# Kernel optimization log

Hardware: AMD Instinct MI355X
Metric: run time of the kernel (lower is better)

Reference implementation:

```python
import jax, jax.numpy as jnp
import numpy as np

B, S, D, H = 2, 2048, 1024, 16
HD = D // H

def setup_inputs() -> dict:
    key = jax.random.key(0)
    ks = jax.random.split(key, 9)
    scale = 1.0 / np.sqrt(D)
    return {
        "query": jax.random.normal(ks[0], (B, S, D), jnp.float32),
        "key":   jax.random.normal(ks[1], (B, S, D), jnp.float32),
        "value": jax.random.normal(ks[2], (B, S, D), jnp.float32),
        "Wq_w": jax.random.normal(ks[3], (D, D), jnp.float32) * scale,
        "Wq_b": jax.random.normal(ks[4], (D,), jnp.float32) * scale,
        "Wk_w": jax.random.normal(ks[5], (D, D), jnp.float32) * scale,
        "Wk_b": jax.random.normal(ks[6], (D,), jnp.float32) * scale,
        "Wv_w": jax.random.normal(ks[7], (D, D), jnp.float32) * scale,
        "Wv_b": jax.random.normal(ks[8], (D,), jnp.float32) * scale,
    }

def reference(query, key, value, Wq_w, Wq_b, Wk_w, Wk_b, Wv_w, Wv_b):
    b, s, d = query.shape
    # torch Linear: y = x @ W.T + b
    Q = query @ Wq_w.T + Wq_b
    K = key   @ Wk_w.T + Wk_b
    V = value @ Wv_w.T + Wv_b
    # [B, H, S, HD]
    Q = Q.reshape(b, -1, H, HD).transpose(0, 2, 1, 3)
    K = K.reshape(b, -1, H, HD).transpose(0, 2, 1, 3)
    V = V.reshape(b, -1, H, HD).transpose(0, 2, 1, 3)
    scores = jnp.einsum("bhqd,bhkd->bhqk", Q, K) / jnp.sqrt(jnp.float32(HD))
    attn = jax.nn.softmax(scores, axis=-1)
    context = jnp.einsum("bhqk,bhkd->bhqd", attn, V)  # [B,H,S,HD]
    attn_output = context.transpose(0, 2, 1, 3).reshape(b, -1, H * HD)  # [B,S,D]
    return (context, attn_output)
```

## Files before the change

### kernel.cpp

```cpp
#include <hip/hip_runtime.h>
#include <hip/hip_bf16.h>

constexpr int Bb = 2, Ss = 2048, Dd = 1024, Hh = 16, HD = 64;
constexpr int Mrows = Bb * Ss;
constexpr float QSCALE = 0.125f * 1.44269504088896f;
constexpr size_t CTX_ELEMS = (size_t)Bb * Hh * Ss * HD;

typedef __attribute__((ext_vector_type(8)))  short        short8;
typedef __attribute__((ext_vector_type(4)))  float        floatx4;
typedef __attribute__((ext_vector_type(16))) float        floatx16;
typedef __attribute__((ext_vector_type(4)))  unsigned int uintx4;
typedef __attribute__((ext_vector_type(8)))  __bf16       bf16x8;

#define DEVI __device__ __forceinline__

DEVI unsigned short f2bf(float f) {
  union { float f; unsigned u; } x; x.f = f;
  return (unsigned short)((x.u + 0x7fffu + ((x.u >> 16) & 1u)) >> 16);
}
DEVI float fexp2(float x) {
#if __has_builtin(__builtin_amdgcn_exp2f)
  return __builtin_amdgcn_exp2f(x);
#else
  return __expf(x * 0.6931471805599453f);
#endif
}
DEVI unsigned int cvtpk(float lo, float hi) {
  unsigned int r;
  asm("v_cvt_pk_bf16_f32 %0, %1, %2" : "=v"(r) : "v"(lo), "v"(hi));
  return r;
}

constexpr size_t XE = (size_t)Mrows * Dd;
constexpr size_t WE = (size_t)Dd * Dd;
constexpr size_t OFF_O = 3 * WE;

__global__ __launch_bounds__(256) void convert_w(
    const float* __restrict__ wq, const float* __restrict__ wk, const float* __restrict__ wv,
    unsigned short* __restrict__ dst)
{
  const int sel = blockIdx.y;
  const float* src = sel == 0 ? wq : sel == 1 ? wk : wv;
  unsigned short* d = dst + (size_t)sel * WE;
  const size_t stride = (size_t)gridDim.x * blockDim.x;
  for (size_t i = (size_t)blockIdx.x * blockDim.x + threadIdx.x; i < WE / 8; i += stride) {
    const floatx4 a = *(const floatx4*)(src + i * 8);
    const floatx4 b = *(const floatx4*)(src + i * 8 + 4);
    uintx4 o;
    o[0] = cvtpk(a[0], a[1]); o[1] = cvtpk(a[2], a[3]);
    o[2] = cvtpk(b[0], b[1]); o[3] = cvtpk(b[2], b[3]);
    *(uintx4*)(d + i * 8) = o;
  }
}

template<bool SWAP>
DEVI void store_out(floatx4 (&acc)[4][4], const float* __restrict__ bias,
                    unsigned short* __restrict__ out, float oscale,
                    int bm, int bn, int wm, int wn, int lrow, int lg)
{
  if constexpr (!SWAP) {
    #pragma unroll
    for (int ni = 0; ni < 4; ++ni) {
      const int gcol = bn * 128 + wn + ni * 16 + lrow;
      const float bval = bias[gcol];
      const int h = gcol >> 6, hd = gcol & 63;
      #pragma unroll
      for (int mi = 0; mi < 4; ++mi)
        #pragma unroll
        for (int r = 0; r < 4; ++r) {
          const int grow = bm * 128 + wm + mi * 16 + lg * 4 + r;
          const int b = grow >> 11, s = grow & 2047;
          out[(((size_t)(b * Hh + h) * Ss + s) << 6) + hd] = f2bf((acc[mi][ni][r] + bval) * oscale);
        }
    }
  } else {
    #pragma unroll
    for (int ni = 0; ni < 4; ++ni)
      #pragma unroll
      for (int r = 0; r < 4; ++r) {
        const int n = bn * 128 + wn + ni * 16 + lg * 4 + r;
        const float bval = bias[n];
        #pragma unroll
        for (int mi = 0; mi < 4; ++mi) {
          const int m = bm * 128 + wm + mi * 16 + lrow;
          out[(size_t)n * Mrows + m] = f2bf(acc[mi][ni][r] + bval);
        }
      }
  }
}

DEVI void gload16(const unsigned short* g, unsigned short* l) {
  __builtin_amdgcn_global_load_lds(
      (const __attribute__((address_space(1))) unsigned int*)g,
      (__attribute__((address_space(3))) unsigned int*)l, 16, 0, 0);
}

template<bool SWAP>
DEVI void gemm_core_mixed(const float* __restrict__ X,
                          const unsigned short* __restrict__ W,
                          const float* __restrict__ bias,
                          unsigned short* __restrict__ out, float oscale,
                          unsigned short* As, unsigned short* Bs, int bm, int bn)
{
  const int t = threadIdx.x, wid = t >> 6, lane = t & 63;
  const int lrow = lane & 15, lg = lane >> 4;
  const int wm = (wid >> 1) * 64, wn = (wid & 1) * 64;

  const int ar = t >> 2;
  const int acb = (t & 3) * 16;
  const float* gAbase = X + (size_t)(bm * 128 + ar) * Dd + acb;

  const int srow = lane >> 3;
  const int gch  = (lane & 7) ^ srow;
  const unsigned short* gB = W + (size_t)(bn * 128 + wid * 32 + srow) * Dd + gch * 8;
  unsigned short* lB = Bs + wid * 4 * 512;

  floatx4 ra[2][4];
  auto loadA = [&](int k0) {
    #pragma unroll
    for (int i = 0; i < 2; ++i)
      #pragma unroll
      for (int j = 0; j < 4; ++j)
        ra[i][j] = *(const floatx4*)(gAbase + (size_t)i * 64 * Dd + k0 + j * 4);
  };
  auto writeA = [&]() {
    #pragma unroll
    for (int i = 0; i < 2; ++i) {
      const int row = ar + i * 64;
      #pragma unroll
      for (int j2 = 0; j2 < 2; ++j2) {
        const floatx4 a = ra[i][2 * j2], b = ra[i][2 * j2 + 1];
        uintx4 w;
        w[0] = cvtpk(a[0], a[1]); w[1] = cvtpk(a[2], a[3]);
        w[2] = cvtpk(b[0], b[1]); w[3] = cvtpk(b[2], b[3]);
        const int cc = (acb >> 3) + j2;
        *(uintx4*)&As[row * 64 + ((cc ^ (row & 7)) << 3)] = w;
      }
    }
  };

  floatx4 acc[4][4];
  #pragma unroll
  for (int i = 0; i < 4; ++i)
    #pragma unroll
    for (int j = 0; j < 4; ++j) acc[i][j] = 0.0f;

  loadA(0);

  for (int k0 = 0; k0 < Dd; k0 += 64) {
    __syncthreads();
    writeA();
    #pragma unroll
    for (int j = 0; j < 4; ++j)
      gload16(gB + (size_t)j * 8 * Dd + k0, lB + j * 512);
    __syncthreads();
    if (k0 + 64 < Dd) loadA(k0 + 64);

    #pragma unroll
    for (int kf = 0; kf < 2; ++kf) {
      bf16x8 af[4], bf[4];
      #pragma unroll
      for (int mi = 0; mi < 4; ++mi) {
        const int row = wm + mi * 16 + lrow;
        const int ch  = ((kf << 2) | lg) ^ (lrow & 7);
        af[mi] = __builtin_bit_cast(bf16x8, *(const short8*)&As[row * 64 + (ch << 3)]);
      }
      #pragma unroll
      for (int ni = 0; ni < 4; ++ni) {
        const int row = wn + ni * 16 + lrow;
        const int ch  = ((kf << 2) | lg) ^ (lrow & 7);
        bf[ni] = __builtin_bit_cast(bf16x8, *(const short8*)&Bs[row * 64 + (ch << 3)]);
      }
      #pragma unroll
      for (int mi = 0; mi < 4; ++mi)
        #pragma unroll
        for (int ni = 0; ni < 4; ++ni) {
          if constexpr (SWAP)
            acc[mi][ni] = __builtin_amdgcn_mfma_f32_16x16x32_bf16(bf[ni], af[mi], acc[mi][ni], 0, 0, 0);
          else
            acc[mi][ni] = __builtin_amdgcn_mfma_f32_16x16x32_bf16(af[mi], bf[ni], acc[mi][ni], 0, 0, 0);
        }
    }
  }
  store_out<SWAP>(acc, bias, out, oscale, bm, bn, wm, wn, lrow, lg);
}

__global__ __launch_bounds__(256, 3) void qkv_gemm(
    const float* __restrict__ q, const float* __restrict__ k, const float* __restrict__ v,
    const unsigned short* __restrict__ wbf,
    const float* __restrict__ bq, const float* __restrict__ bk, const float* __restrict__ bv,
    unsigned short* __restrict__ outbase)
{
  __shared__ __align__(16) unsigned short As[128 * 64];
  __shared__ __align__(16) unsigned short Bs[128 * 64];

  const int id  = blockIdx.y * 256 + blockIdx.x;
  const int swz = (id & 7) * 96 + (id >> 3);
  const int sel = swz >> 8;
  const int bx  = swz & 255;
  const int bm = bx >> 3, bn = bx & 7;

  const float* X = sel == 0 ? q : sel == 1 ? k : v;
  const unsigned short* W = wbf + (size_t)sel * WE;
  const float* bias = sel == 0 ? bq : sel == 1 ? bk : bv;
  unsigned short* out = outbase + (size_t)sel * XE;

  if (sel == 2) gemm_core_mixed<true >(X, W, bias, out, 1.0f, As, Bs, bm, bn);
  else          gemm_core_mixed<false>(X, W, bias, out, sel == 0 ? QSCALE : 1.0f, As, Bs, bm, bn);
}

__global__ __launch_bounds__(512, 4) void attn_fwd8(
    const unsigned short* __restrict__ Qw, const unsigned short* __restrict__ Kw,
    const unsigned short* __restrict__ Vw, float* __restrict__ out)
{
  __shared__ __align__(16) char smemRaw[65536];
  unsigned short* KsB = (unsigned short*)smemRaw;
  unsigned short* VtB = (unsigned short*)(smemRaw + 32768);
  float* ctxL  = (float*)smemRaw;
  float* lsumL = (float*)(smemRaw + 32768);

  const int id  = blockIdx.y * 16 + blockIdx.x;
  const int swz = (id & 7) * 64 + (id >> 3);
  const int qb  = swz & 15, bh = swz >> 4;
  const int b   = bh >> 4, h = bh & 15;

  const int t = threadIdx.x, wid8 = t >> 6, lane = t & 63;
  const int kh = wid8 >> 2, wid = wid8 & 3;
  const int l31 = lane & 31, hi = lane >> 5;
  const int kvbase = kh << 10;
  const unsigned short* Qb = Qw + (size_t)bh * (Ss * HD);
  const unsigned short* Kb = Kw + (size_t)bh * (Ss * HD);
  const unsigned short* Vg = Vw + (size_t)(h * 64) * Mrows + b * Ss;
  const int q0 = qb * 128 + wid * 32;

  bf16x8 qf[4];
  #pragma unroll
  for (int hs = 0; hs < 4; ++hs)
    qf[hs] = __builtin_bit_cast(bf16x8,
        *(const short8*)(Qb + (size_t)(q0 + l31) * 64 + hs * 16 + hi * 8));

  floatx16 ctx[2];
  ctx[0] = 0.0f; ctx[1] = 0.0f;
  float lsumv = 0.0f;

  const int rl = lane >> 3;
  const int cs = (lane & 7) ^ rl;
  auto stage = [&](int T) {
    const int kv0 = kvbase + T * 64;
    unsigned short* Kd = KsB + (size_t)(kh * 2 + (T & 1)) * 4096;
    unsigned short* Vd = VtB + (size_t)(kh * 2 + (T & 1)) * 4096;
    #pragma unroll
    for (int i = 0; i < 2; ++i) {
      const int row = wid * 16 + i * 8 + rl;
      gload16(Kb + (size_t)(kv0 + row) * 64 + cs * 8, Kd + (wid * 16 + i * 8) * 64);
      gload16(Vg + (size_t)row * Mrows + kv0 + cs * 8, Vd + (wid * 16 + i * 8) * 64);
    }
  };

  stage(0);

  for (int it = 0; it < 16; ++it) {
    const int cur = it & 1;
    __syncthreads();
    if (it + 1 < 16) stage(it + 1);
    const unsigned short* Kc = KsB + (size_t)(kh * 2 + cur) * 4096;
    const unsigned short* Vc = VtB + (size_t)(kh * 2 + cur) * 4096;

    #pragma unroll
    for (int kvb = 0; kvb < 2; ++kvb) {
      floatx16 s = 0.0f;
      __builtin_amdgcn_s_setprio(1);
      #pragma unroll
      for (int hs = 0; hs < 4; ++hs) {
        const int ch = ((hs << 1) | hi) ^ (l31 & 7);
        const bf16x8 kf = __builtin_bit_cast(bf16x8,
            *(const short8*)&Kc[(kvb * 32 + l31) * 64 + (ch << 3)]);
        s = __builtin_amdgcn_mfma_f32_32x32x16_bf16(kf, qf[hs], s, 0, 0, 0);
      }
      __builtin_amdgcn_s_setprio(0);

      float p[16];
      #pragma unroll
      for (int r = 0; r < 16; ++r) { p[r] = fexp2(s[r]); lsumv += p[r]; }
      unsigned int c[8];
      #pragma unroll
      for (int i = 0; i < 8; ++i)
        asm("v_cvt_pk_bf16_f32 %0, %1, %2" : "=v"(c[i]) : "v"(p[2 * i]), "v"(p[2 * i + 1]));

      #pragma unroll
      for (int ks2 = 0; ks2 < 2; ++ks2) {
        unsigned int w0 = c[4 * ks2 + 0], w2 = c[4 * ks2 + 2];
        unsigned int w1 = c[4 * ks2 + 1], w3 = c[4 * ks2 + 3];
        asm("v_permlane32_swap_b32 %0, %1" : "+v"(w0), "+v"(w2));
        asm("v_permlane32_swap_b32 %0, %1" : "+v"(w1), "+v"(w3));
        uintx4 paw; paw[0] = w0; paw[1] = w1; paw[2] = w2; paw[3] = w3;
        const bf16x8 pa = __builtin_bit_cast(bf16x8, paw);

        const int ks = kvb * 2 + ks2;
        __builtin_amdgcn_s_setprio(1);
        #pragma unroll
        for (int nb = 0; nb < 2; ++nb) {
          const int ch = ((ks << 1) | hi) ^ (l31 & 7);
          const bf16x8 vf = __builtin_bit_cast(bf16x8,
              *(const short8*)&Vc[(nb * 32 + l31) * 64 + (ch << 3)]);
          ctx[nb] = __builtin_amdgcn_mfma_f32_32x32x16_bf16(pa, vf, ctx[nb], 0, 0, 0);
        }
        __builtin_amdgcn_s_setprio(0);
      }
    }
  }

  float sa = lsumv, sb = lsumv;
  asm("v_permlane32_swap_b32 %0, %1" : "+v"(sa), "+v"(sb));
  const float tot = lsumv + (hi ? sa : sb);

  __syncthreads();
  if (kh == 1) {
    #pragma unroll
    for (int r = 0; r < 16; ++r)
      #pragma unroll
      for (int nb = 0; nb < 2; ++nb)
        ctxL[(nb * 16 + r) * 256 + wid * 64 + lane] = ctx[nb][r];
    if (hi == 0) lsumL[wid * 32 + l31] = tot;
  }
  __syncthreads();
  if (kh == 0) {
    if (hi == 0) lsumL[128 + wid * 32 + l31] = tot + lsumL[wid * 32 + l31];
    #pragma unroll
    for (int r = 0; r < 16; ++r) {
      const int wr = (r & 3) + 8 * (r >> 2) + 4 * hi;
      const float inv = 1.0f / lsumL[128 + wid * 32 + wr];
      const int qrow = q0 + wr;
      #pragma unroll
      for (int nb = 0; nb < 2; ++nb) {
        const int hd = nb * 32 + l31;
        const float val = (ctx[nb][r] + ctxL[(nb * 16 + r) * 256 + wid * 64 + lane]) * inv;
        out[((size_t)bh * Ss + qrow) * 64 + hd] = val;
        out[CTX_ELEMS + (((size_t)(b * Ss + qrow)) << 10) + (h << 6) + hd] = val;
      }
    }
  }
}

extern "C" void kernel_launch(void* const* d_in, const int* in_sizes, int n_in,
                              void* d_out, int out_size, void* d_ws, size_t ws_size,
                              hipStream_t stream) {
  const float* q  = (const float*)d_in[0];
  const float* k  = (const float*)d_in[1];
  const float* v  = (const float*)d_in[2];
  const float* wq = (const float*)d_in[3];
  const float* bq = (const float*)d_in[4];
  const float* wk = (const float*)d_in[5];
  const float* bk = (const float*)d_in[6];
  const float* wv = (const float*)d_in[7];
  const float* bv = (const float*)d_in[8];
  unsigned short* ws = (unsigned short*)d_ws;
  float* out = (float*)d_out;

  unsigned short* wsW = ws;
  unsigned short* wsO = ws + OFF_O;

  convert_w<<<dim3(64, 3), 256, 0, stream>>>(wq, wk, wv, wsW);
  qkv_gemm<<<dim3(256, 3), 256, 0, stream>>>(q, k, v, wsW, bq, bk, bv, wsO);
  attn_fwd8<<<dim3(16, 32), 512, 0, stream>>>(wsO, wsO + XE, wsO + 2 * XE, out);
}
```

Measured before the change: 89.76 us.

## Pre-convert activations to bf16 and split attention KV into four quarters

The convert kernel now casts the q/k/v activations to bf16 along with the weights, so the QKV GEMM can load both operands straight into LDS with async global_load_lds instead of loading fp32 and converting in registers. The attention kernel now handles 64 query rows per block with four KV-quarter wave pairs, uses smaller LDS tiles (single-buffered K, double-buffered V) and a four-way reduction at the end, and launches twice as many blocks with a higher occupancy hint. This trades an extra full pass over the activations in the convert step for a simpler GEMM inner loop and more parallelism in attention.

```diff
diff --git a/kernel.cpp b/kernel.cpp
--- a/kernel.cpp
+++ b/kernel.cpp
@@ -25,31 +25,36 @@
   return __expf(x * 0.6931471805599453f);
 #endif
 }
-DEVI unsigned int cvtpk(float lo, float hi) {
-  unsigned int r;
-  asm("v_cvt_pk_bf16_f32 %0, %1, %2" : "=v"(r) : "v"(lo), "v"(hi));
-  return r;
-}
 
 constexpr size_t XE = (size_t)Mrows * Dd;
 constexpr size_t WE = (size_t)Dd * Dd;
-constexpr size_t OFF_O = 3 * WE;
-
-__global__ __launch_bounds__(256) void convert_w(
+constexpr size_t OFF_W = 3 * XE;
+constexpr size_t OFF_O = 3 * XE + 3 * WE;
+
+__global__ __launch_bounds__(256) void convert_bf16(
+    const float* __restrict__ q, const float* __restrict__ k, const float* __restrict__ v,
     const float* __restrict__ wq, const float* __restrict__ wk, const float* __restrict__ wv,
     unsigned short* __restrict__ dst)
 {
   const int sel = blockIdx.y;
-  const float* src = sel == 0 ? wq : sel == 1 ? wk : wv;
-  unsigned short* d = dst + (size_t)sel * WE;
+  const float* src; size_t n, off;
+  switch (sel) {
+    case 0:  src = q;  n = XE; off = 0;            break;
+    case 1:  src = k;  n = XE; off = XE;           break;
+    case 2:  src = v;  n = XE; off = 2 * XE;       break;
+    case 3:  src = wq; n = WE; off = OFF_W;        break;
+    case 4:  src = wk; n = WE; off = OFF_W + WE;   break;
+    default: src = wv; n = WE; off = OFF_W + 2*WE; break;
+  }
+  unsigned short* d = dst + off;
   const size_t stride = (size_t)gridDim.x * blockDim.x;
-  for (size_t i = (size_t)blockIdx.x * blockDim.x + threadIdx.x; i < WE / 8; i += stride) {
+  for (size_t i = (size_t)blockIdx.x * blockDim.x + threadIdx.x; i < n / 8; i += stride) {
     const floatx4 a = *(const floatx4*)(src + i * 8);
     const floatx4 b = *(const floatx4*)(src + i * 8 + 4);
-    uintx4 o;
-    o[0] = cvtpk(a[0], a[1]); o[1] = cvtpk(a[2], a[3]);
-    o[2] = cvtpk(b[0], b[1]); o[3] = cvtpk(b[2], b[3]);
-    *(uintx4*)(d + i * 8) = o;
+    short8 o;
+    #pragma unroll
+    for (int j = 0; j < 4; ++j) { o[j] = (short)f2bf(a[j]); o[4 + j] = (short)f2bf(b[j]); }
+    *(short8*)(d + i * 8) = o;
   }
 }
 
@@ -96,48 +101,22 @@
 }
 
 template<bool SWAP>
-DEVI void gemm_core_mixed(const float* __restrict__ X,
-                          const unsigned short* __restrict__ W,
-                          const float* __restrict__ bias,
-                          unsigned short* __restrict__ out, float oscale,
-                          unsigned short* As, unsigned short* Bs, int bm, int bn)
+DEVI void gemm_core_bf16(const unsigned short* __restrict__ X,
+                         const unsigned short* __restrict__ W,
+                         const float* __restrict__ bias,
+                         unsigned short* __restrict__ out, float oscale,
+                         unsigned short* As, unsigned short* Bs, int bm, int bn)
 {
   const int t = threadIdx.x, wid = t >> 6, lane = t & 63;
   const int lrow = lane & 15, lg = lane >> 4;
   const int wm = (wid >> 1) * 64, wn = (wid & 1) * 64;
 
-  const int ar = t >> 2;
-  const int acb = (t & 3) * 16;
-  const float* gAbase = X + (size_t)(bm * 128 + ar) * Dd + acb;
-
   const int srow = lane >> 3;
   const int gch  = (lane & 7) ^ srow;
+  const unsigned short* gA = X + (size_t)(bm * 128 + wid * 32 + srow) * Dd + gch * 8;
   const unsigned short* gB = W + (size_t)(bn * 128 + wid * 32 + srow) * Dd + gch * 8;
+  unsigned short* lA = As + wid * 4 * 512;
   unsigned short* lB = Bs + wid * 4 * 512;
-
-  floatx4 ra[2][4];
-  auto loadA = [&](int k0) {
-    #pragma unroll
-    for (int i = 0; i < 2; ++i)
-      #pragma unroll
-      for (int j = 0; j < 4; ++j)
-        ra[i][j] = *(const floatx4*)(gAbase + (size_t)i * 64 * Dd + k0 + j * 4);
-  };
-  auto writeA = [&]() {
-    #pragma unroll
-    for (int i = 0; i < 2; ++i) {
-      const int row = ar + i * 64;
-      #pragma unroll
-      for (int j2 = 0; j2 < 2; ++j2) {
-        const floatx4 a = ra[i][2 * j2], b = ra[i][2 * j2 + 1];
-        uintx4 w;
-        w[0] = cvtpk(a[0], a[1]); w[1] = cvtpk(a[2], a[3]);
-        w[2] = cvtpk(b[0], b[1]); w[3] = cvtpk(b[2], b[3]);
-        const int cc = (acb >> 3) + j2;
-        *(uintx4*)&As[row * 64 + ((cc ^ (row & 7)) << 3)] = w;
-      }
-    }
-  };
 
   floatx4 acc[4][4];
   #pragma unroll
@@ -145,16 +124,14 @@
     #pragma unroll
     for (int j = 0; j < 4; ++j) acc[i][j] = 0.0f;
 
-  loadA(0);
-
   for (int k0 = 0; k0 < Dd; k0 += 64) {
     __syncthreads();
-    writeA();
-    #pragma unroll
-    for (int j = 0; j < 4; ++j)
+    #pragma unroll
+    for (int j = 0; j < 4; ++j) {
+      gload16(gA + (size_t)j * 8 * Dd + k0, lA + j * 512);
       gload16(gB + (size_t)j * 8 * Dd + k0, lB + j * 512);
+    }
     __syncthreads();
-    if (k0 + 64 < Dd) loadA(k0 + 64);
 
     #pragma unroll
     for (int kf = 0; kf < 2; ++kf) {
@@ -185,9 +162,8 @@
   store_out<SWAP>(acc, bias, out, oscale, bm, bn, wm, wn, lrow, lg);
 }
 
-__global__ __launch_bounds__(256, 3) void qkv_gemm(
-    const float* __restrict__ q, const float* __restrict__ k, const float* __restrict__ v,
-    const unsigned short* __restrict__ wbf,
+__global__ __launch_bounds__(256, 3) void qkv_gemm_bf16(
+    const unsigned short* __restrict__ ws,
     const float* __restrict__ bq, const float* __restrict__ bk, const float* __restrict__ bv,
     unsigned short* __restrict__ outbase)
 {
@@ -200,38 +176,40 @@
   const int bx  = swz & 255;
   const int bm = bx >> 3, bn = bx & 7;
 
-  const float* X = sel == 0 ? q : sel == 1 ? k : v;
-  const unsigned short* W = wbf + (size_t)sel * WE;
+  const unsigned short* X = ws + (size_t)sel * XE;
+  const unsigned short* W = ws + OFF_W + (size_t)sel * WE;
   const float* bias = sel == 0 ? bq : sel == 1 ? bk : bv;
   unsigned short* out = outbase + (size_t)sel * XE;
 
-  if (sel == 2) gemm_core_mixed<true >(X, W, bias, out, 1.0f, As, Bs, bm, bn);
-  else          gemm_core_mixed<false>(X, W, bias, out, sel == 0 ? QSCALE : 1.0f, As, Bs, bm, bn);
-}
-
-__global__ __launch_bounds__(512, 4) void attn_fwd8(
+  if (sel == 2) gemm_core_bf16<true >(X, W, bias, out, 1.0f,   As, Bs, bm, bn);
+  else          gemm_core_bf16<false>(X, W, bias, out, sel == 0 ? QSCALE : 1.0f, As, Bs, bm, bn);
+}
+
+__global__ __launch_bounds__(512, 6) void attn_fwd8(
     const unsigned short* __restrict__ Qw, const unsigned short* __restrict__ Kw,
     const unsigned short* __restrict__ Vw, float* __restrict__ out)
 {
-  __shared__ __align__(16) char smemRaw[65536];
-  unsigned short* KsB = (unsigned short*)smemRaw;
-  unsigned short* VtB = (unsigned short*)(smemRaw + 32768);
-  float* ctxL  = (float*)smemRaw;
-  float* lsumL = (float*)(smemRaw + 32768);
-
-  const int id  = blockIdx.y * 16 + blockIdx.x;
-  const int swz = (id & 7) * 64 + (id >> 3);
-  const int qb  = swz & 15, bh = swz >> 4;
+  __shared__ __align__(16) char smemRaw[50176];
+  float* ctxF  = (float*)smemRaw;
+  float* lsumQ = (float*)(smemRaw + 49152);
+  float* lsumC = (float*)(smemRaw + 49152 + 768);
+
+  const int id  = blockIdx.y * 32 + blockIdx.x;
+  const int swz = (id & 7) * 128 + (id >> 3);
+  const int qb  = swz & 31, bh = swz >> 5;
   const int b   = bh >> 4, h = bh & 15;
 
   const int t = threadIdx.x, wid8 = t >> 6, lane = t & 63;
-  const int kh = wid8 >> 2, wid = wid8 & 3;
+  const int kq = wid8 >> 1, wid = wid8 & 1;
   const int l31 = lane & 31, hi = lane >> 5;
-  const int kvbase = kh << 10;
+  const int kvbase = kq << 9;
   const unsigned short* Qb = Qw + (size_t)bh * (Ss * HD);
   const unsigned short* Kb = Kw + (size_t)bh * (Ss * HD);
   const unsigned short* Vg = Vw + (size_t)(h * 64) * Mrows + b * Ss;
-  const int q0 = qb * 128 + wid * 32;
+  const int q0 = qb * 64 + wid * 32;
+
+  unsigned short* Kq = (unsigned short*)(smemRaw + kq * 4096);
+  unsigned short* Vq = (unsigned short*)(smemRaw + 16384 + kq * 8192);
 
   bf16x8 qf[4];
   #pragma unroll
@@ -245,68 +223,77 @@
 
   const int rl = lane >> 3;
   const int cs = (lane & 7) ^ rl;
-  auto stage = [&](int T) {
-    const int kv0 = kvbase + T * 64;
-    unsigned short* Kd = KsB + (size_t)(kh * 2 + (T & 1)) * 4096;
-    unsigned short* Vd = VtB + (size_t)(kh * 2 + (T & 1)) * 4096;
+  auto stageK = [&](int T) {
+    const int kv0 = kvbase + T * 32;
     #pragma unroll
     for (int i = 0; i < 2; ++i) {
       const int row = wid * 16 + i * 8 + rl;
-      gload16(Kb + (size_t)(kv0 + row) * 64 + cs * 8, Kd + (wid * 16 + i * 8) * 64);
-      gload16(Vg + (size_t)row * Mrows + kv0 + cs * 8, Vd + (wid * 16 + i * 8) * 64);
+      gload16(Kb + (size_t)(kv0 + row) * 64 + cs * 8, Kq + (wid * 16 + i * 8) * 64);
     }
   };
-
-  stage(0);
-
-  for (int it = 0; it < 16; ++it) {
-    const int cur = it & 1;
+  const int rv = lane >> 2;
+  const int cv = (lane & 3) ^ (rv & 3);
+  auto stageV = [&](int T) {
+    const int kv0 = kvbase + T * 32;
+    unsigned short* Vd = Vq + (T & 1) * 2048;
+    #pragma unroll
+    for (int i = 0; i < 2; ++i) {
+      const int rowb = wid * 32 + i * 16;
+      gload16(Vg + (size_t)(rowb + rv) * Mrows + kv0 + cv * 8, Vd + rowb * 32);
+    }
+  };
+
+  stageV(0);
+  stageK(0);
+
+  for (int T = 0; T < 16; ++T) {
     __syncthreads();
-    if (it + 1 < 16) stage(it + 1);
-    const unsigned short* Kc = KsB + (size_t)(kh * 2 + cur) * 4096;
-    const unsigned short* Vc = VtB + (size_t)(kh * 2 + cur) * 4096;
-
-    #pragma unroll
-    for (int kvb = 0; kvb < 2; ++kvb) {
-      floatx16 s = 0.0f;
+    if (T + 1 < 16) stageV(T + 1);
+    const unsigned short* Vc = Vq + (T & 1) * 2048;
+
+    floatx16 s = 0.0f;
+    __builtin_amdgcn_s_setprio(1);
+    #pragma unroll
+    for (int hs = 0; hs < 4; ++hs) {
+      const int ch = ((hs << 1) | hi) ^ (l31 & 7);
+      const bf16x8 kf = __builtin_bit_cast(bf16x8,
+          *(const short8*)&Kq[l31 * 64 + (ch << 3)]);
+      s = __builtin_amdgcn_mfma_f32_32x32x16_bf16(kf, qf[hs], s, 0, 0, 0);
+    }
+    __builtin_amdgcn_s_setprio(0);
+
+    if (T + 1 < 16) {
+      __syncthreads();
+      stageK(T + 1);
+    }
+
+    float p[16];
+    #pragma unroll
+    for (int r = 0; r < 16; ++r) { p[r] = fexp2(s[r]); lsumv += p[r]; }
+    unsigned int c[8];
+    #pragma unroll
+    for (int i = 0; i < 8; ++i)
+      asm("v_cvt_pk_bf16_f32 %0, %1, %2" : "=v"(c[i]) : "v"(p[2 * i]), "v"(p[2 * i + 1]));
+
+    #pragma unroll
+    for (int ks2 = 0; ks2 < 2; ++ks2) {
+      unsigned int w0 = c[4 * ks2 + 0], w2 = c[4 * ks2 + 2];
+      unsigned int w1 = c[4 * ks2 + 1], w3 = c[4 * ks2 + 3];
+      asm("v_permlane32_swap_b32 %0, %1" : "+v"(w0), "+v"(w2));
+      asm("v_permlane32_swap_b32 %0, %1" : "+v"(w1), "+v"(w3));
+      uintx4 paw; paw[0] = w0; paw[1] = w1; paw[2] = w2; paw[3] = w3;
+      const bf16x8 pa = __builtin_bit_cast(bf16x8, paw);
+
       __builtin_amdgcn_s_setprio(1);
       #pragma unroll
-      for (int hs = 0; hs < 4; ++hs) {
-        const int ch = ((hs << 1) | hi) ^ (l31 & 7);
-        const bf16x8 kf = __builtin_bit_cast(bf16x8,
-            *(const short8*)&Kc[(kvb * 32 + l31) * 64 + (ch << 3)]);
-        s = __builtin_amdgcn_mfma_f32_32x32x16_bf16(kf, qf[hs], s, 0, 0, 0);
+      for (int nb = 0; nb < 2; ++nb) {
+        const int r = nb * 32 + l31;
+        const int ch = ((ks2 << 1) | hi) ^ (l31 & 3);
+        const bf16x8 vf = __builtin_bit_cast(bf16x8,
+            *(const short8*)&Vc[r * 32 + (ch << 3)]);
+        ctx[nb] = __builtin_amdgcn_mfma_f32_32x32x16_bf16(pa, vf, ctx[nb], 0, 0, 0);
       }
       __builtin_amdgcn_s_setprio(0);
-
-      float p[16];
-      #pragma unroll
-      for (int r = 0; r < 16; ++r) { p[r] = fexp2(s[r]); lsumv += p[r]; }
-      unsigned int c[8];
-      #pragma unroll
-      for (int i = 0; i < 8; ++i)
-        asm("v_cvt_pk_bf16_f32 %0, %1, %2" : "=v"(c[i]) : "v"(p[2 * i]), "v"(p[2 * i + 1]));
-
-      #pragma unroll
-      for (int ks2 = 0; ks2 < 2; ++ks2) {
-        unsigned int w0 = c[4 * ks2 + 0], w2 = c[4 * ks2 + 2];
-        unsigned int w1 = c[4 * ks2 + 1], w3 = c[4 * ks2 + 3];
-        asm("v_permlane32_swap_b32 %0, %1" : "+v"(w0), "+v"(w2));
-        asm("v_permlane32_swap_b32 %0, %1" : "+v"(w1), "+v"(w3));
-        uintx4 paw; paw[0] = w0; paw[1] = w1; paw[2] = w2; paw[3] = w3;
-        const bf16x8 pa = __builtin_bit_cast(bf16x8, paw);
-
-        const int ks = kvb * 2 + ks2;
-        __builtin_amdgcn_s_setprio(1);
-        #pragma unroll
-        for (int nb = 0; nb < 2; ++nb) {
-          const int ch = ((ks << 1) | hi) ^ (l31 & 7);
-          const bf16x8 vf = __builtin_bit_cast(bf16x8,
-              *(const short8*)&Vc[(nb * 32 + l31) * 64 + (ch << 3)]);
-          ctx[nb] = __builtin_amdgcn_mfma_f32_32x32x16_bf16(pa, vf, ctx[nb], 0, 0, 0);
-        }
-        __builtin_amdgcn_s_setprio(0);
-      }
     }
   }
 
@@ -315,26 +302,33 @@
   const float tot = lsumv + (hi ? sa : sb);
 
   __syncthreads();
-  if (kh == 1) {
+  if (kq != 0) {
+    const int sl = (kq - 1) * 2 + wid;
     #pragma unroll
     for (int r = 0; r < 16; ++r)
       #pragma unroll
       for (int nb = 0; nb < 2; ++nb)
-        ctxL[(nb * 16 + r) * 256 + wid * 64 + lane] = ctx[nb][r];
-    if (hi == 0) lsumL[wid * 32 + l31] = tot;
+        ctxF[sl * 2048 + (nb * 16 + r) * 64 + lane] = ctx[nb][r];
+    if (hi == 0) lsumQ[sl * 32 + l31] = tot;
   }
   __syncthreads();
-  if (kh == 0) {
-    if (hi == 0) lsumL[128 + wid * 32 + l31] = tot + lsumL[wid * 32 + l31];
+  if (kq == 0) {
+    if (hi == 0)
+      lsumC[wid * 32 + l31] = tot + lsumQ[wid * 32 + l31]
+                                  + lsumQ[(2 + wid) * 32 + l31]
+                                  + lsumQ[(4 + wid) * 32 + l31];
     #pragma unroll
     for (int r = 0; r < 16; ++r) {
       const int wr = (r & 3) + 8 * (r >> 2) + 4 * hi;
-      const float inv = 1.0f / lsumL[128 + wid * 32 + wr];
+      const float inv = 1.0f / lsumC[wid * 32 + wr];
       const int qrow = q0 + wr;
       #pragma unroll
       for (int nb = 0; nb < 2; ++nb) {
         const int hd = nb * 32 + l31;
-        const float val = (ctx[nb][r] + ctxL[(nb * 16 + r) * 256 + wid * 64 + lane]) * inv;
+        const float val = (ctx[nb][r]
+                           + ctxF[(0 + wid) * 2048 + (nb * 16 + r) * 64 + lane]
+                           + ctxF[(2 + wid) * 2048 + (nb * 16 + r) * 64 + lane]
+                           + ctxF[(4 + wid) * 2048 + (nb * 16 + r) * 64 + lane]) * inv;
         out[((size_t)bh * Ss + qrow) * 64 + hd] = val;
         out[CTX_ELEMS + (((size_t)(b * Ss + qrow)) << 10) + (h << 6) + hd] = val;
       }
@@ -357,10 +351,8 @@
   unsigned short* ws = (unsigned short*)d_ws;
   float* out = (float*)d_out;
 
-  unsigned short* wsW = ws;
-  unsigned short* wsO = ws + OFF_O;
-
-  convert_w<<<dim3(64, 3), 256, 0, stream>>>(wq, wk, wv, wsW);
-  qkv_gemm<<<dim3(256, 3), 256, 0, stream>>>(q, k, v, wsW, bq, bk, bv, wsO);
-  attn_fwd8<<<dim3(16, 32), 512, 0, stream>>>(wsO, wsO + XE, wsO + 2 * XE, out);
-}
+  convert_bf16<<<dim3(256, 6), 256, 0, stream>>>(q, k, v, wq, wk, wv, ws);
+  qkv_gemm_bf16<<<dim3(256, 3), 256, 0, stream>>>(ws, bq, bk, bv, ws + OFF_O);
+  attn_fwd8<<<dim3(32, 32), 512, 0, stream>>>(
+      ws + OFF_O, ws + OFF_O + XE, ws + OFF_O + 2 * XE, out);
+}
```

Result: slower. 144.3 us (+60.8%).
